# Kernel optimization log

Measured on AMD Instinct MI355X. Metric: run time of the kernel, lower is better.

Reference implementation:

```python
import jax, jax.numpy as jnp
import numpy as np

SOBEL_X = jnp.array([[-1.0, 0.0, 1.0], [-2.0, 0.0, 2.0], [-1.0, 0.0, 1.0]], dtype=jnp.float32).reshape(1, 1, 3, 3)
SOBEL_Y = jnp.array([[-1.0, -2.0, -1.0], [0.0, 0.0, 0.0], [1.0, 2.0, 1.0]], dtype=jnp.float32).reshape(1, 1, 3, 3)
EPS = 1e-05


def setup_inputs() -> dict:
    key = jax.random.key(0)
    x = jax.random.uniform(key, (32, 1, 1024, 1024), dtype=jnp.float32)
    return {"x": x}


def _conv3x3(x, k):
    # NCHW input, OIHW kernel, stride 1, SAME padding (padding=1 for 3x3)
    return jax.lax.conv_general_dilated(
        x, k, window_strides=(1, 1), padding=((1, 1), (1, 1)),
        dimension_numbers=("NCHW", "OIHW", "NCHW"))


def reference(x) -> jnp.ndarray:
    grad_x = _conv3x3(x, SOBEL_X)
    grad_y = _conv3x3(x, SOBEL_Y)
    return jnp.abs(grad_x) + jnp.abs(grad_y) + EPS
```

## Files before the change

### kernel.cpp

```cpp
#include <hip/hip_runtime.h>
#include <hip/hip_bf16.h>


#define W 1024
#define H 1024
#define R 16
#define EPS 1e-5f

typedef float v4f __attribute__((ext_vector_type(4)));

__device__ __forceinline__ void loadrow(const float* __restrict__ base, int y,
                                        int x0, float* dst) {
    if (y < 0 || y >= H) {
        dst[0] = dst[1] = dst[2] = dst[3] = dst[4] = dst[5] = 0.f;
        return;
    }
    const float* r = base + (size_t)y * W;
    v4f v = *(const v4f*)(r + x0);
    dst[1] = v.x; dst[2] = v.y; dst[3] = v.z; dst[4] = v.w;
    dst[0] = (x0 > 0) ? r[x0 - 1] : 0.f;
    dst[5] = (x0 + 4 < W) ? r[x0 + 4] : 0.f;
}

__global__ __launch_bounds__(256) void sobel_kernel(const float* __restrict__ in,
                                                    float* __restrict__ out) {
    const int b = blockIdx.x;
    const int t = ((b & 255) << 3) | (b >> 8);
    const int img = t >> 6;
    const int ty = (t & 63) * R;
    const int x0 = threadIdx.x << 2;

    const float* base = in + (size_t)img * (W * H);
    float* obase = out + (size_t)img * (W * H);

    float T[6], M[6], B[6], Nx[6];
    loadrow(base, ty - 1, x0, T);
    loadrow(base, ty,     x0, M);
    loadrow(base, ty + 1, x0, B);

#pragma unroll 4
    for (int i = 0; i < R; ++i) {
        const int y = ty + i;
        loadrow(base, y + 2, x0, Nx);

        v4f o;
#pragma unroll
        for (int j = 0; j < 4; ++j) {
            float gx = (T[j + 2] - T[j]) + 2.0f * (M[j + 2] - M[j]) + (B[j + 2] - B[j]);
            float gy = (B[j] + 2.0f * B[j + 1] + B[j + 2]) - (T[j] + 2.0f * T[j + 1] + T[j + 2]);
            o[j] = fabsf(gx) + fabsf(gy) + EPS;
        }
        __builtin_nontemporal_store(o, (v4f*)(obase + (size_t)y * W + x0));

#pragma unroll
        for (int j = 0; j < 6; ++j) { T[j] = M[j]; M[j] = B[j]; B[j] = Nx[j]; }
    }
}

extern "C" void kernel_launch(void* const* d_in, const int* in_sizes, int n_in,
                              void* d_out, int out_size, void* d_ws, size_t ws_size,
                              hipStream_t stream) {
    const float* x = (const float*)d_in[0];
    float* out = (float*)d_out;
    const int N = 32;
    dim3 grid(N * (H / R));
    dim3 block(256);
    sobel_kernel<<<grid, block, 0, stream>>>(x, out);
}
```

Before: 236.8 us.

## Prefetch rows through a six-deep register ring with unaligned vector halo loads

```diff
diff --git a/kernel.cpp b/kernel.cpp
--- a/kernel.cpp
+++ b/kernel.cpp
@@ -1,59 +1,84 @@
 #include <hip/hip_runtime.h>
-#include <hip/hip_bf16.h>
 
 
 #define W 1024
 #define H 1024
 #define R 16
+#define NR 6
 #define EPS 1e-5f
 
 typedef float v4f __attribute__((ext_vector_type(4)));
+typedef float v2f __attribute__((ext_vector_type(2)));
+typedef v4f v4f_u __attribute__((aligned(4)));
+typedef v2f v2f_u __attribute__((aligned(4)));
 
-__device__ __forceinline__ void loadrow(const float* __restrict__ base, int y,
-                                        int x0, float* dst) {
-    if (y < 0 || y >= H) {
-        dst[0] = dst[1] = dst[2] = dst[3] = dst[4] = dst[5] = 0.f;
-        return;
+__device__ __forceinline__ void issue_row(const float* __restrict__ base, int y,
+                                          int xl, int xr, float* s) {
+    if ((unsigned)y < (unsigned)H) {
+        const float* r = base + (size_t)y * W;
+        v4f a = *(const v4f_u*)(r + xl);
+        v2f b = *(const v2f_u*)(r + xr);
+        s[0] = a.x; s[1] = a.y; s[2] = a.z; s[3] = a.w;
+        s[4] = b.x; s[5] = b.y;
+    } else {
+        s[0] = s[1] = s[2] = s[3] = s[4] = s[5] = 0.f;
     }
-    const float* r = base + (size_t)y * W;
-    v4f v = *(const v4f*)(r + x0);
-    dst[1] = v.x; dst[2] = v.y; dst[3] = v.z; dst[4] = v.w;
-    dst[0] = (x0 > 0) ? r[x0 - 1] : 0.f;
-    dst[5] = (x0 + 4 < W) ? r[x0 + 4] : 0.f;
 }
 
-__global__ __launch_bounds__(256) void sobel_kernel(const float* __restrict__ in,
-                                                    float* __restrict__ out) {
+__device__ __forceinline__ void fix_edges(float* s, bool t0, bool tN) {
+    float n3 = t0 ? s[2] : s[3];
+    float n2 = t0 ? s[1] : s[2];
+    float n1 = t0 ? s[0] : s[1];
+    float n0 = t0 ? 0.f  : s[0];
+    s[0] = n0; s[1] = n1; s[2] = n2; s[3] = n3;
+    float n4 = tN ? s[5] : s[4];
+    float n5 = tN ? 0.f  : s[5];
+    s[4] = n4; s[5] = n5;
+}
+
+__global__ __launch_bounds__(256, 8) void sobel_kernel(const float* __restrict__ in,
+                                                       float* __restrict__ out) {
     const int b = blockIdx.x;
     const int t = ((b & 255) << 3) | (b >> 8);
     const int img = t >> 6;
     const int ty = (t & 63) * R;
     const int x0 = threadIdx.x << 2;
 
-    const float* base = in + (size_t)img * (W * H);
-    float* obase = out + (size_t)img * (W * H);
+    const int  xl = (x0 == 0)     ? 0       : x0 - 1;
+    const int  xr = (x0 == W - 4) ? (W - 2) : x0 + 3;
+    const bool t0 = (x0 == 0);
+    const bool tN = (x0 == W - 4);
 
-    float T[6], M[6], B[6], Nx[6];
-    loadrow(base, ty - 1, x0, T);
-    loadrow(base, ty,     x0, M);
-    loadrow(base, ty + 1, x0, B);
+    const float* base  = in  + (size_t)img * (W * H);
+    float*       obase = out + (size_t)img * (W * H);
 
-#pragma unroll 4
+    float rs[NR][6];
+
+#pragma unroll
+    for (int k = 0; k < NR; ++k)
+        issue_row(base, ty - 1 + k, xl, xr, rs[k]);
+    fix_edges(rs[0], t0, tN);
+    fix_edges(rs[1], t0, tN);
+
+#pragma unroll
     for (int i = 0; i < R; ++i) {
-        const int y = ty + i;
-        loadrow(base, y + 2, x0, Nx);
+        fix_edges(rs[(i + 2) % NR], t0, tN);
+
+        float* Tr = rs[(i + 0) % NR];
+        float* Mr = rs[(i + 1) % NR];
+        float* Br = rs[(i + 2) % NR];
 
         v4f o;
 #pragma unroll
         for (int j = 0; j < 4; ++j) {
-            float gx = (T[j + 2] - T[j]) + 2.0f * (M[j + 2] - M[j]) + (B[j + 2] - B[j]);
-            float gy = (B[j] + 2.0f * B[j + 1] + B[j + 2]) - (T[j] + 2.0f * T[j + 1] + T[j + 2]);
+            float gx = (Tr[j + 2] - Tr[j]) + 2.0f * (Mr[j + 2] - Mr[j]) + (Br[j + 2] - Br[j]);
+            float gy = (Br[j] + 2.0f * Br[j + 1] + Br[j + 2]) - (Tr[j] + 2.0f * Tr[j + 1] + Tr[j + 2]);
             o[j] = fabsf(gx) + fabsf(gy) + EPS;
         }
-        __builtin_nontemporal_store(o, (v4f*)(obase + (size_t)y * W + x0));
+        __builtin_nontemporal_store(o, (v4f*)(obase + (size_t)(ty + i) * W + x0));
 
-#pragma unroll
-        for (int j = 0; j < 6; ++j) { T[j] = M[j]; M[j] = B[j]; B[j] = Nx[j]; }
+        if (i + 5 <= R)
+            issue_row(base, ty + i + 5, xl, xr, rs[i % NR]);
     }
 }
 
@@ -61,9 +86,9 @@
                               void* d_out, int out_size, void* d_ws, size_t ws_size,
                               hipStream_t stream) {
     const float* x = (const float*)d_in[0];
-    float* out = (float*)d_out;
+    float* outp = (float*)d_out;
     const int N = 32;
     dim3 grid(N * (H / R));
     dim3 block(256);
-    sobel_kernel<<<grid, block, 0, stream>>>(x, out);
+    sobel_kernel<<<grid, block, 0, stream>>>(x, outp);
 }
```

Result: no change. 233.5 us (-1.4%).

## Stage input rows through LDS with async global-to-LDS loads ring buffer

Applied to the files above, without the earlier changes.

```diff
diff --git a/kernel.cpp b/kernel.cpp
--- a/kernel.cpp
+++ b/kernel.cpp
@@ -1,59 +1,101 @@
 #include <hip/hip_runtime.h>
-#include <hip/hip_bf16.h>
 
 
 #define W 1024
 #define H 1024
 #define R 16
+#define NB 5
 #define EPS 1e-5f
 
 typedef float v4f __attribute__((ext_vector_type(4)));
 
-__device__ __forceinline__ void loadrow(const float* __restrict__ base, int y,
-                                        int x0, float* dst) {
-    if (y < 0 || y >= H) {
-        dst[0] = dst[1] = dst[2] = dst[3] = dst[4] = dst[5] = 0.f;
-        return;
-    }
-    const float* r = base + (size_t)y * W;
-    v4f v = *(const v4f*)(r + x0);
-    dst[1] = v.x; dst[2] = v.y; dst[3] = v.z; dst[4] = v.w;
-    dst[0] = (x0 > 0) ? r[x0 - 1] : 0.f;
-    dst[5] = (x0 + 4 < W) ? r[x0 + 4] : 0.f;
-}
+#define WAITVM(n)                                          \
+    do {                                                   \
+        asm volatile("s_waitcnt vmcnt(" #n ")" ::: "memory"); \
+        __builtin_amdgcn_sched_barrier(0);                 \
+    } while (0)
 
-__global__ __launch_bounds__(256) void sobel_kernel(const float* __restrict__ in,
-                                                    float* __restrict__ out) {
+#define GLOAD_LDS16(g, l)                                                     \
+    __builtin_amdgcn_global_load_lds(                                         \
+        (const __attribute__((address_space(1))) void*)(g),                   \
+        (__attribute__((address_space(3))) void*)(l), 16, 0, 0)
+
+__global__ __launch_bounds__(256, 8) void sobel_kernel(const float* __restrict__ in,
+                                                       float* __restrict__ out) {
+    __shared__ float lds[NB * W];
+
     const int b = blockIdx.x;
     const int t = ((b & 255) << 3) | (b >> 8);
     const int img = t >> 6;
     const int ty = (t & 63) * R;
-    const int x0 = threadIdx.x << 2;
+    const int tid = threadIdx.x;
+    const int x0 = tid << 2;
+    const int wave = tid >> 6;
 
-    const float* base = in + (size_t)img * (W * H);
-    float* obase = out + (size_t)img * (W * H);
+    const bool t0 = (tid == 0);
+    const bool tN = (tid == 255);
+    const int cl = t0 ? 0 : (x0 - 4);
+    const int cr = tN ? x0 : (x0 + 4);
 
-    float T[6], M[6], B[6], Nx[6];
-    loadrow(base, ty - 1, x0, T);
-    loadrow(base, ty,     x0, M);
-    loadrow(base, ty + 1, x0, B);
+    const float* base  = in  + (size_t)img * (W * H);
+    float*       obase = out + (size_t)img * (W * H);
 
-#pragma unroll 4
+    auto dma = [&](int y, int s) {
+        const int yc = (y < 0) ? 0 : ((y > H - 1) ? (H - 1) : y);
+        const float* g = base + (size_t)yc * W + x0;
+        GLOAD_LDS16(g, lds + s * W + (wave << 8));
+    };
+
+    auto ldrow = [&](int s, float* d, bool zero) {
+        const float* p = lds + s * W;
+        v4f A = *(const v4f*)(p + cl);
+        v4f M = *(const v4f*)(p + x0);
+        v4f C = *(const v4f*)(p + cr);
+        float l = t0 ? 0.f : A.w;
+        float r = tN ? 0.f : C.x;
+        d[0] = zero ? 0.f : l;
+        d[1] = zero ? 0.f : M.x;
+        d[2] = zero ? 0.f : M.y;
+        d[3] = zero ? 0.f : M.z;
+        d[4] = zero ? 0.f : M.w;
+        d[5] = zero ? 0.f : r;
+    };
+
+    dma(ty - 1, 0);
+    dma(ty,     1);
+    dma(ty + 1, 2);
+    dma(ty + 2, 3);
+
+    WAITVM(2);
+    __builtin_amdgcn_s_barrier();
+
+    float Tw[6], Mw[6], Bw[6];
+    ldrow(0, Tw, ty == 0);
+    ldrow(1, Mw, false);
+
+#pragma unroll
     for (int i = 0; i < R; ++i) {
-        const int y = ty + i;
-        loadrow(base, y + 2, x0, Nx);
+        if (i == 0)            WAITVM(1);
+        else if (i == 1)       WAITVM(2);
+        else if (i == R - 1)   WAITVM(2);
+        else                   WAITVM(3);
+        __builtin_amdgcn_s_barrier();
+
+        if (i <= R - 3) dma(ty + i + 3, (i + 4) % NB);
+
+        ldrow((i + 2) % NB, Bw, ty + i + 1 >= H);
 
         v4f o;
 #pragma unroll
         for (int j = 0; j < 4; ++j) {
-            float gx = (T[j + 2] - T[j]) + 2.0f * (M[j + 2] - M[j]) + (B[j + 2] - B[j]);
-            float gy = (B[j] + 2.0f * B[j + 1] + B[j + 2]) - (T[j] + 2.0f * T[j + 1] + T[j + 2]);
+            float gx = (Tw[j + 2] - Tw[j]) + 2.0f * (Mw[j + 2] - Mw[j]) + (Bw[j + 2] - Bw[j]);
+            float gy = (Bw[j] + 2.0f * Bw[j + 1] + Bw[j + 2]) - (Tw[j] + 2.0f * Tw[j + 1] + Tw[j + 2]);
             o[j] = fabsf(gx) + fabsf(gy) + EPS;
         }
-        __builtin_nontemporal_store(o, (v4f*)(obase + (size_t)y * W + x0));
+        __builtin_nontemporal_store(o, (v4f*)(obase + (size_t)(ty + i) * W + x0));
 
 #pragma unroll
-        for (int j = 0; j < 6; ++j) { T[j] = M[j]; M[j] = B[j]; B[j] = Nx[j]; }
+        for (int j = 0; j < 6; ++j) { Tw[j] = Mw[j]; Mw[j] = Bw[j]; }
     }
 }
 
@@ -61,9 +103,9 @@
                               void* d_out, int out_size, void* d_ws, size_t ws_size,
                               hipStream_t stream) {
     const float* x = (const float*)d_in[0];
-    float* out = (float*)d_out;
+    float* outp = (float*)d_out;
     const int N = 32;
     dim3 grid(N * (H / R));
     dim3 block(256);
-    sobel_kernel<<<grid, block, 0, stream>>>(x, out);
+    sobel_kernel<<<grid, block, 0, stream>>>(x, outp);
 }
```

Result: no change. 234.5 us (-1.0%).

## Software-pipeline row loads with inline asm and explicit vmcnt waits

Applied to the files above, without the earlier changes.

```diff
diff --git a/kernel.cpp b/kernel.cpp
--- a/kernel.cpp
+++ b/kernel.cpp
@@ -1,5 +1,4 @@
 #include <hip/hip_runtime.h>
-#include <hip/hip_bf16.h>
 
 
 #define W 1024
@@ -9,61 +8,110 @@
 
 typedef float v4f __attribute__((ext_vector_type(4)));
 
-__device__ __forceinline__ void loadrow(const float* __restrict__ base, int y,
-                                        int x0, float* dst) {
-    if (y < 0 || y >= H) {
-        dst[0] = dst[1] = dst[2] = dst[3] = dst[4] = dst[5] = 0.f;
-        return;
-    }
-    const float* r = base + (size_t)y * W;
-    v4f v = *(const v4f*)(r + x0);
-    dst[1] = v.x; dst[2] = v.y; dst[3] = v.z; dst[4] = v.w;
-    dst[0] = (x0 > 0) ? r[x0 - 1] : 0.f;
-    dst[5] = (x0 + 4 < W) ? r[x0 + 4] : 0.f;
-}
+#define WAITVM(n)                                             \
+    do {                                                      \
+        asm volatile("s_waitcnt vmcnt(" #n ")" ::: "memory"); \
+        __builtin_amdgcn_sched_barrier(0);                    \
+    } while (0)
 
-__global__ __launch_bounds__(256) void sobel_kernel(const float* __restrict__ in,
-                                                    float* __restrict__ out) {
+__global__ __launch_bounds__(256, 6) void sobel_kernel(const float* __restrict__ in,
+                                                       float* __restrict__ out) {
     const int b = blockIdx.x;
     const int t = ((b & 255) << 3) | (b >> 8);
     const int img = t >> 6;
     const int ty = (t & 63) * R;
-    const int x0 = threadIdx.x << 2;
+    const int tid = threadIdx.x;
+    const int x0 = tid << 2;
 
-    const float* base = in + (size_t)img * (W * H);
-    float* obase = out + (size_t)img * (W * H);
+    const bool t0 = (tid == 0);
+    const bool tN = (tid == 255);
+    const unsigned offM = (unsigned)(x0 << 2);
+    const unsigned offL = t0 ? 0u : (unsigned)((x0 << 2) - 4);
+    const unsigned offR = tN ? 4092u : (unsigned)((x0 << 2) + 16);
 
-    float T[6], M[6], B[6], Nx[6];
-    loadrow(base, ty - 1, x0, T);
-    loadrow(base, ty,     x0, M);
-    loadrow(base, ty + 1, x0, B);
+    const unsigned long long base =
+        (unsigned long long)(in + (size_t)img * (size_t)(W * H));
+    float* obase = out + (size_t)img * (size_t)(W * H);
 
-#pragma unroll 4
+    v4f   fm[5];
+    float fl[5];
+    float fr[5];
+
+#define ISSUE(yy, s)                                                     \
+    do {                                                                 \
+        int yc_ = (yy);                                                  \
+        yc_ = yc_ < 0 ? 0 : (yc_ > H - 1 ? H - 1 : yc_);                 \
+        const unsigned ro_ = (unsigned)yc_ << 12;                        \
+        asm volatile("global_load_dwordx4 %0, %1, %2"                    \
+                     : "=v"(fm[s]) : "v"(ro_ + offM), "s"(base) : "memory"); \
+        asm volatile("global_load_dword %0, %1, %2"                      \
+                     : "=v"(fl[s]) : "v"(ro_ + offL), "s"(base) : "memory"); \
+        asm volatile("global_load_dword %0, %1, %2"                      \
+                     : "=v"(fr[s]) : "v"(ro_ + offR), "s"(base) : "memory"); \
+    } while (0)
+
+#define CONSUME(s, zero, d)                                              \
+    do {                                                                 \
+        const v4f   m_ = fm[s];                                          \
+        const float l_ = fl[s];                                          \
+        const float r_ = fr[s];                                          \
+        const bool  z_ = (zero);                                         \
+        d[0] = (z_ || t0) ? 0.f : l_;                                    \
+        d[1] = z_ ? 0.f : m_.x;                                          \
+        d[2] = z_ ? 0.f : m_.y;                                          \
+        d[3] = z_ ? 0.f : m_.z;                                          \
+        d[4] = z_ ? 0.f : m_.w;                                          \
+        d[5] = (z_ || tN) ? 0.f : r_;                                    \
+    } while (0)
+
+    ISSUE(ty - 1, 0);
+    ISSUE(ty,     1);
+    ISSUE(ty + 1, 2);
+    ISSUE(ty + 2, 3);
+    ISSUE(ty + 3, 4);
+
+    WAITVM(9);
+    float Tw[6], Mw[6], Bw[6];
+    CONSUME(0, ty == 0, Tw);
+    CONSUME(1, false,   Mw);
+
+#pragma unroll
     for (int i = 0; i < R; ++i) {
         const int y = ty + i;
-        loadrow(base, y + 2, x0, Nx);
+
+        if (i == 0)       WAITVM(6);
+        else if (i == 1)  WAITVM(7);
+        else if (i <= 13) WAITVM(8);
+        else if (i == 14) WAITVM(6);
+        else              WAITVM(3);
+
+        CONSUME((i + 2) % 5, y + 1 >= H, Bw);
+
+        if (i <= 12) ISSUE(y + 4, i % 5);
 
         v4f o;
 #pragma unroll
         for (int j = 0; j < 4; ++j) {
-            float gx = (T[j + 2] - T[j]) + 2.0f * (M[j + 2] - M[j]) + (B[j + 2] - B[j]);
-            float gy = (B[j] + 2.0f * B[j + 1] + B[j + 2]) - (T[j] + 2.0f * T[j + 1] + T[j + 2]);
+            float gx = (Tw[j + 2] - Tw[j]) + 2.0f * (Mw[j + 2] - Mw[j]) + (Bw[j + 2] - Bw[j]);
+            float gy = (Bw[j] + 2.0f * Bw[j + 1] + Bw[j + 2]) - (Tw[j] + 2.0f * Tw[j + 1] + Tw[j + 2]);
             o[j] = fabsf(gx) + fabsf(gy) + EPS;
         }
-        __builtin_nontemporal_store(o, (v4f*)(obase + (size_t)y * W + x0));
+        *(v4f*)(obase + (size_t)y * W + x0) = o;
 
 #pragma unroll
-        for (int j = 0; j < 6; ++j) { T[j] = M[j]; M[j] = B[j]; B[j] = Nx[j]; }
+        for (int j = 0; j < 6; ++j) { Tw[j] = Mw[j]; Mw[j] = Bw[j]; }
     }
+#undef ISSUE
+#undef CONSUME
 }
 
 extern "C" void kernel_launch(void* const* d_in, const int* in_sizes, int n_in,
                               void* d_out, int out_size, void* d_ws, size_t ws_size,
                               hipStream_t stream) {
     const float* x = (const float*)d_in[0];
-    float* out = (float*)d_out;
+    float* outp = (float*)d_out;
     const int N = 32;
     dim3 grid(N * (H / R));
     dim3 block(256);
-    sobel_kernel<<<grid, block, 0, stream>>>(x, out);
+    sobel_kernel<<<grid, block, 0, stream>>>(x, outp);
 }
```

After: 235.3 us. Within noise of the previous version (-0.7%).
